# Optimization experiments

Hardware: AMD Instinct MI355X
Metric: run time of the kernel (lower is better)

Reference implementation:

```python
import jax, jax.numpy as jnp
import numpy as np

N_NODES = 50000
N_EDGES = 800000
D_IN = 128
D_OUT = 128


def setup_inputs() -> dict:
    key = jax.random.key(0)
    ks = jax.random.split(key, 6)
    x = jax.random.normal(ks[0], (N_NODES, D_IN), dtype=jnp.float32)
    edge_src = jax.random.randint(ks[1], (N_EDGES,), 0, N_NODES)
    edge_dst = jax.random.randint(ks[2], (N_EDGES,), 0, N_NODES)
    edge_val = jax.random.uniform(ks[3], (N_EDGES,), dtype=jnp.float32)
    W = jax.random.normal(ks[4], (D_OUT, D_IN), dtype=jnp.float32) / np.sqrt(D_IN)
    b = jax.random.normal(ks[5], (D_OUT,), dtype=jnp.float32) * 0.01
    return {"x": x, "edge_src": edge_src, "edge_dst": edge_dst,
            "edge_val": edge_val, "W": W, "b": b}


def reference(x, edge_src, edge_dst, edge_val, W, b):
    # h = sparse.mm(adj, x): for each edge (dst, src, val): h[dst] += val * x[src]
    msgs = edge_val[:, None] * x[edge_src]            # [E, D_IN]
    h = jax.ops.segment_sum(msgs, edge_dst, num_segments=N_NODES)  # [N, D_IN]
    # nn.Linear: h @ W.T + b, then relu activation
    out = jnp.einsum('nd,od->no', h, W) + b           # [N, D_OUT]
    return jax.nn.relu(out)
```

## Files before the change

kernel.cpp:

```cpp
#include <hip/hip_runtime.h>
#include <hip/hip_bf16.h>

#define N_NODES 50000
#define N_EDGES 800000
#define D 128
#define SCAN_NB 49

static_assert(N_NODES < 65536, "src must fit in 16 bits for epack");

typedef __attribute__((ext_vector_type(8))) short short8;
typedef __attribute__((ext_vector_type(4))) float f32x4;
typedef unsigned int uint;
typedef unsigned short ushort;

__device__ __forceinline__ ushort f2bf(float f) {
    uint u = __float_as_uint(f);
    u += 0x7fffu + ((u >> 16) & 1u);
    return (ushort)(u >> 16);
}

__device__ __forceinline__ float bflo(uint u) { return __uint_as_float(u << 16); }
__device__ __forceinline__ float bfhi(uint u) { return __uint_as_float(u & 0xffff0000u); }


__global__ __launch_bounds__(256) void sgcn_prep(
    const float* __restrict__ W, ushort* __restrict__ Wb, int* __restrict__ deg)
{
    int t = blockIdx.x * 256 + threadIdx.x;
    if (t < (D * D) / 4) {
        float4 a = reinterpret_cast<const float4*>(W)[t];
        ushort4 s;
        s.x = f2bf(a.x); s.y = f2bf(a.y); s.z = f2bf(a.z); s.w = f2bf(a.w);
        *reinterpret_cast<ushort4*>(Wb + (size_t)t * 4) = s;
    }
    if (t < N_NODES / 4) {
        reinterpret_cast<int4*>(deg)[t] = make_int4(0, 0, 0, 0);
    }
}


__global__ __launch_bounds__(256) void sgcn_hist_rank(
    const int* __restrict__ dst, int* __restrict__ deg, int* __restrict__ rank)
{
    int e = blockIdx.x * 256 + threadIdx.x;
    if (e < N_EDGES)
        rank[e] = atomicAdd(&deg[dst[e]], 1);
}

__global__ __launch_bounds__(256) void sgcn_scanf(
    const int* __restrict__ deg, int* __restrict__ rowptr)
{
    __shared__ int part[256];
    __shared__ int soff;
    int tid = threadIdx.x;
    int b = blockIdx.x;

    const int4* d4 = reinterpret_cast<const int4*>(deg);
    int pre = 0;
    for (int i = tid; i < b * 256; i += 256) {
        int4 v = d4[i];
        pre += v.x + v.y + v.z + v.w;
    }
    part[tid] = pre;
    __syncthreads();
    for (int off = 128; off > 0; off >>= 1) {
        if (tid < off) part[tid] += part[tid + off];
        __syncthreads();
    }
    if (tid == 0) soff = part[0];
    __syncthreads();

    int base = b * 1024 + tid * 4;
    int4 v = make_int4(0, 0, 0, 0);
    if (base < N_NODES) v = *reinterpret_cast<const int4*>(deg + base);
    int s = v.x + v.y + v.z + v.w;
    part[tid] = s;
    __syncthreads();
    for (int off = 1; off < 256; off <<= 1) {
        int mine  = part[tid];
        int other = (tid >= off) ? part[tid - off] : 0;
        __syncthreads();
        part[tid] = mine + other;
        __syncthreads();
    }
    int run = soff + ((tid == 0) ? 0 : part[tid - 1]);
    if (base < N_NODES) {
        int4 r;
        r.x = run;
        r.y = run + v.x;
        r.z = r.y + v.y;
        r.w = r.z + v.z;
        *reinterpret_cast<int4*>(rowptr + base) = r;
        if (base + 4 == N_NODES) rowptr[N_NODES] = r.w + v.w;
    }
}

__global__ __launch_bounds__(256) void sgcn_permute(
    const int* __restrict__ src, const int* __restrict__ dst,
    const float* __restrict__ val, const int* __restrict__ rowptr,
    const int* __restrict__ rank, uint* __restrict__ epack)
{
    int e = blockIdx.x * 256 + threadIdx.x;
    if (e < N_EDGES) {
        int pos = rowptr[dst[e]] + rank[e];
        epack[pos] = ((uint)f2bf(val[e]) << 16) | (uint)src[e];
    }
}


__global__ __launch_bounds__(256) void sgcn_gemm_y(
    const float* __restrict__ x, const ushort* __restrict__ Wb,
    ushort* __restrict__ y)
{
    int wave = threadIdx.x >> 6;
    int lane = threadIdx.x & 63;
    int lm = lane & 15;
    int kb = lane >> 4;

    short8 bfr[8][4];
#pragma unroll
    for (int nt = 0; nt < 8; ++nt)
#pragma unroll
        for (int kk = 0; kk < 4; ++kk)
            bfr[nt][kk] = *reinterpret_cast<const short8*>(
                Wb + (nt * 16 + lm) * D + kk * 32 + kb * 8);

    const int nMT = N_NODES / 16;
    int mt0 = blockIdx.x * 4 + wave;
    int strideMT = gridDim.x * 4;
    for (int mt = mt0; mt < nMT; mt += strideMT) {
        int m0 = mt * 16;
        const float* xrow = x + (long)(m0 + lm) * D + kb * 8;
        short8 afr[4];
#pragma unroll
        for (int kk = 0; kk < 4; ++kk) {
            float4 a = *reinterpret_cast<const float4*>(xrow + kk * 32);
            float4 c = *reinterpret_cast<const float4*>(xrow + kk * 32 + 4);
            short8 s;
            s[0] = (short)f2bf(a.x); s[1] = (short)f2bf(a.y);
            s[2] = (short)f2bf(a.z); s[3] = (short)f2bf(a.w);
            s[4] = (short)f2bf(c.x); s[5] = (short)f2bf(c.y);
            s[6] = (short)f2bf(c.z); s[7] = (short)f2bf(c.w);
            afr[kk] = s;
        }
#pragma unroll
        for (int nt = 0; nt < 8; ++nt) {
            f32x4 acc = {0.f, 0.f, 0.f, 0.f};
#pragma unroll
            for (int kk = 0; kk < 4; ++kk)
                acc = __builtin_amdgcn_mfma_f32_16x16x32_bf16(afr[kk], bfr[nt][kk], acc, 0, 0, 0);
            ushort* yp = y + (long)(m0 + kb * 4) * D + nt * 16 + lm;
#pragma unroll
            for (int r = 0; r < 4; ++r)
                yp[(long)r * D] = f2bf(acc[r]);
        }
    }
}


__global__ __launch_bounds__(256) void sgcn_aggregate(
    const uint* __restrict__ yb, const int* __restrict__ rowptr,
    const uint* __restrict__ ep, const float* __restrict__ bias,
    float* __restrict__ out)
{
    int n = (blockIdx.x * 256 + threadIdx.x) >> 4;
    int c = threadIdx.x & 15;
    float4 bv0 = *reinterpret_cast<const float4*>(bias + c * 8);
    float4 bv1 = *reinterpret_cast<const float4*>(bias + c * 8 + 4);

    int j0 = rowptr[n], j1 = rowptr[n + 1];
    float a0 = 0.f, a1 = 0.f, a2 = 0.f, a3 = 0.f;
    float a4 = 0.f, a5 = 0.f, a6 = 0.f, a7 = 0.f;
    int j = j0;
    for (; j + 4 <= j1; j += 4) {
        uint p0 = ep[j], p1 = ep[j + 1], p2 = ep[j + 2], p3 = ep[j + 3];
        uint4 u0 = *reinterpret_cast<const uint4*>(yb + (size_t)(p0 & 0xffffu) * 64 + c * 4);
        uint4 u1 = *reinterpret_cast<const uint4*>(yb + (size_t)(p1 & 0xffffu) * 64 + c * 4);
        uint4 u2 = *reinterpret_cast<const uint4*>(yb + (size_t)(p2 & 0xffffu) * 64 + c * 4);
        uint4 u3 = *reinterpret_cast<const uint4*>(yb + (size_t)(p3 & 0xffffu) * 64 + c * 4);
        float v0 = __uint_as_float(p0 & 0xffff0000u);
        float v1 = __uint_as_float(p1 & 0xffff0000u);
        float v2 = __uint_as_float(p2 & 0xffff0000u);
        float v3 = __uint_as_float(p3 & 0xffff0000u);
        a0 += v0 * bflo(u0.x) + v1 * bflo(u1.x) + v2 * bflo(u2.x) + v3 * bflo(u3.x);
        a1 += v0 * bfhi(u0.x) + v1 * bfhi(u1.x) + v2 * bfhi(u2.x) + v3 * bfhi(u3.x);
        a2 += v0 * bflo(u0.y) + v1 * bflo(u1.y) + v2 * bflo(u2.y) + v3 * bflo(u3.y);
        a3 += v0 * bfhi(u0.y) + v1 * bfhi(u1.y) + v2 * bfhi(u2.y) + v3 * bfhi(u3.y);
        a4 += v0 * bflo(u0.z) + v1 * bflo(u1.z) + v2 * bflo(u2.z) + v3 * bflo(u3.z);
        a5 += v0 * bfhi(u0.z) + v1 * bfhi(u1.z) + v2 * bfhi(u2.z) + v3 * bfhi(u3.z);
        a6 += v0 * bflo(u0.w) + v1 * bflo(u1.w) + v2 * bflo(u2.w) + v3 * bflo(u3.w);
        a7 += v0 * bfhi(u0.w) + v1 * bfhi(u1.w) + v2 * bfhi(u2.w) + v3 * bfhi(u3.w);
    }
    for (; j < j1; ++j) {
        uint p = ep[j];
        uint4 u = *reinterpret_cast<const uint4*>(yb + (size_t)(p & 0xffffu) * 64 + c * 4);
        float v = __uint_as_float(p & 0xffff0000u);
        a0 += v * bflo(u.x); a1 += v * bfhi(u.x);
        a2 += v * bflo(u.y); a3 += v * bfhi(u.y);
        a4 += v * bflo(u.z); a5 += v * bfhi(u.z);
        a6 += v * bflo(u.w); a7 += v * bfhi(u.w);
    }
    f32x4 r0, r1;
    r0[0] = fmaxf(a0 + bv0.x, 0.f);
    r0[1] = fmaxf(a1 + bv0.y, 0.f);
    r0[2] = fmaxf(a2 + bv0.z, 0.f);
    r0[3] = fmaxf(a3 + bv0.w, 0.f);
    r1[0] = fmaxf(a4 + bv1.x, 0.f);
    r1[1] = fmaxf(a5 + bv1.y, 0.f);
    r1[2] = fmaxf(a6 + bv1.z, 0.f);
    r1[3] = fmaxf(a7 + bv1.w, 0.f);
    f32x4* op = reinterpret_cast<f32x4*>(out + (long)n * D + c * 8);
    __builtin_nontemporal_store(r0, op);
    __builtin_nontemporal_store(r1, op + 1);
}

extern "C" void kernel_launch(void* const* d_in, const int* in_sizes, int n_in,
                              void* d_out, int out_size, void* d_ws, size_t ws_size,
                              hipStream_t stream) {
    const float* x   = (const float*)d_in[0];
    const int*   es  = (const int*)d_in[1];
    const int*   ed  = (const int*)d_in[2];
    const float* ev  = (const float*)d_in[3];
    const float* W   = (const float*)d_in[4];
    const float* b   = (const float*)d_in[5];
    float* out = (float*)d_out;

    char* ws = (char*)d_ws;
    size_t off = 0;
    uint*   yb     = (uint*)  (ws + off); off += (size_t)N_NODES * (D / 2) * sizeof(uint);
    ushort* Wb     = (ushort*)(ws + off); off += (size_t)D * D * sizeof(ushort);
    uint*   epack  = (uint*)  (ws + off); off += (size_t)N_EDGES * sizeof(uint);
    int*    rowptr = (int*)   (ws + off); off += ((size_t)(N_NODES + 1) * sizeof(int) + 15) & ~15ull;
    int*    deg    = (int*)   (ws + off); off += (size_t)N_NODES * sizeof(int);
    int* rank = (int*)d_out;

    const int EB = (N_EDGES + 255) / 256;

    sgcn_prep<<<64, 256, 0, stream>>>(W, Wb, deg);
    sgcn_gemm_y<<<512, 256, 0, stream>>>(x, Wb, (ushort*)yb);
    sgcn_hist_rank<<<EB, 256, 0, stream>>>(ed, deg, rank);
    sgcn_scanf<<<SCAN_NB, 256, 0, stream>>>(deg, rowptr);
    sgcn_permute<<<EB, 256, 0, stream>>>(es, ed, ev, rowptr, rank, epack);
    sgcn_aggregate<<<3125, 256, 0, stream>>>(yb, rowptr, epack, b, out);
}
```

Baseline: 115.9 us.

## Fuse GEMM with degree histogram in one launch and convert W in-kernel

Merges the dense x·W GEMM and the edge-degree histogram/rank atomics into a single kernel, with extra blocks doing the histogram so both run concurrently. The separate W-to-bf16 prep kernel is dropped: each GEMM block converts W itself, and deg is zeroed with a memset. Nontemporal loads are added for streaming reads of x, the edge arrays and epack. This cuts the number of launches and lets the atomic-bound and MFMA-bound work overlap, at the cost of redundant W conversion in every GEMM block.

```diff
diff --git a/kernel.cpp b/kernel.cpp
--- a/kernel.cpp
+++ b/kernel.cpp
@@ -5,6 +5,7 @@
 #define N_EDGES 800000
 #define D 128
 #define SCAN_NB 49
+#define GEMM_NB 512
 
 static_assert(N_NODES < 65536, "src must fit in 16 bits for epack");
 
@@ -23,29 +24,71 @@
 __device__ __forceinline__ float bfhi(uint u) { return __uint_as_float(u & 0xffff0000u); }
 
 
-__global__ __launch_bounds__(256) void sgcn_prep(
-    const float* __restrict__ W, ushort* __restrict__ Wb, int* __restrict__ deg)
-{
-    int t = blockIdx.x * 256 + threadIdx.x;
-    if (t < (D * D) / 4) {
-        float4 a = reinterpret_cast<const float4*>(W)[t];
-        ushort4 s;
-        s.x = f2bf(a.x); s.y = f2bf(a.y); s.z = f2bf(a.z); s.w = f2bf(a.w);
-        *reinterpret_cast<ushort4*>(Wb + (size_t)t * 4) = s;
-    }
-    if (t < N_NODES / 4) {
-        reinterpret_cast<int4*>(deg)[t] = make_int4(0, 0, 0, 0);
-    }
-}
-
-
-__global__ __launch_bounds__(256) void sgcn_hist_rank(
-    const int* __restrict__ dst, int* __restrict__ deg, int* __restrict__ rank)
-{
-    int e = blockIdx.x * 256 + threadIdx.x;
-    if (e < N_EDGES)
-        rank[e] = atomicAdd(&deg[dst[e]], 1);
-}
+__global__ __launch_bounds__(256) void sgcn_gemm_hist(
+    const float* __restrict__ x, const float* __restrict__ W,
+    const int* __restrict__ dst, int* __restrict__ deg, int* __restrict__ rank,
+    ushort* __restrict__ y)
+{
+    if (blockIdx.x >= GEMM_NB) {
+        int e = (blockIdx.x - GEMM_NB) * 256 + threadIdx.x;
+        if (e < N_EDGES)
+            rank[e] = atomicAdd(&deg[dst[e]], 1);
+        return;
+    }
+
+    int wave = threadIdx.x >> 6;
+    int lane = threadIdx.x & 63;
+    int lm = lane & 15;
+    int kb = lane >> 4;
+
+    short8 bfr[8][4];
+#pragma unroll
+    for (int nt = 0; nt < 8; ++nt)
+#pragma unroll
+        for (int kk = 0; kk < 4; ++kk) {
+            const float* wp = W + (nt * 16 + lm) * D + kk * 32 + kb * 8;
+            float4 a = *reinterpret_cast<const float4*>(wp);
+            float4 c = *reinterpret_cast<const float4*>(wp + 4);
+            short8 s;
+            s[0] = (short)f2bf(a.x); s[1] = (short)f2bf(a.y);
+            s[2] = (short)f2bf(a.z); s[3] = (short)f2bf(a.w);
+            s[4] = (short)f2bf(c.x); s[5] = (short)f2bf(c.y);
+            s[6] = (short)f2bf(c.z); s[7] = (short)f2bf(c.w);
+            bfr[nt][kk] = s;
+        }
+
+    const int nMT = N_NODES / 16;
+    int mt0 = blockIdx.x * 4 + wave;
+    int strideMT = GEMM_NB * 4;
+    for (int mt = mt0; mt < nMT; mt += strideMT) {
+        int m0 = mt * 16;
+        const float* xrow = x + (long)(m0 + lm) * D + kb * 8;
+        short8 afr[4];
+#pragma unroll
+        for (int kk = 0; kk < 4; ++kk) {
+            f32x4 a = __builtin_nontemporal_load(reinterpret_cast<const f32x4*>(xrow + kk * 32));
+            f32x4 c = __builtin_nontemporal_load(reinterpret_cast<const f32x4*>(xrow + kk * 32 + 4));
+            short8 s;
+            s[0] = (short)f2bf(a[0]); s[1] = (short)f2bf(a[1]);
+            s[2] = (short)f2bf(a[2]); s[3] = (short)f2bf(a[3]);
+            s[4] = (short)f2bf(c[0]); s[5] = (short)f2bf(c[1]);
+            s[6] = (short)f2bf(c[2]); s[7] = (short)f2bf(c[3]);
+            afr[kk] = s;
+        }
+#pragma unroll
+        for (int nt = 0; nt < 8; ++nt) {
+            f32x4 acc = {0.f, 0.f, 0.f, 0.f};
+#pragma unroll
+            for (int kk = 0; kk < 4; ++kk)
+                acc = __builtin_amdgcn_mfma_f32_16x16x32_bf16(afr[kk], bfr[nt][kk], acc, 0, 0, 0);
+            ushort* yp = y + (long)(m0 + kb * 4) * D + nt * 16 + lm;
+#pragma unroll
+            for (int r = 0; r < 4; ++r)
+                yp[(long)r * D] = f2bf(acc[r]);
+        }
+    }
+}
+
 
 __global__ __launch_bounds__(256) void sgcn_scanf(
     const int* __restrict__ deg, int* __restrict__ rowptr)
@@ -102,58 +145,12 @@
 {
     int e = blockIdx.x * 256 + threadIdx.x;
     if (e < N_EDGES) {
-        int pos = rowptr[dst[e]] + rank[e];
-        epack[pos] = ((uint)f2bf(val[e]) << 16) | (uint)src[e];
-    }
-}
-
-
-__global__ __launch_bounds__(256) void sgcn_gemm_y(
-    const float* __restrict__ x, const ushort* __restrict__ Wb,
-    ushort* __restrict__ y)
-{
-    int wave = threadIdx.x >> 6;
-    int lane = threadIdx.x & 63;
-    int lm = lane & 15;
-    int kb = lane >> 4;
-
-    short8 bfr[8][4];
-#pragma unroll
-    for (int nt = 0; nt < 8; ++nt)
-#pragma unroll
-        for (int kk = 0; kk < 4; ++kk)
-            bfr[nt][kk] = *reinterpret_cast<const short8*>(
-                Wb + (nt * 16 + lm) * D + kk * 32 + kb * 8);
-
-    const int nMT = N_NODES / 16;
-    int mt0 = blockIdx.x * 4 + wave;
-    int strideMT = gridDim.x * 4;
-    for (int mt = mt0; mt < nMT; mt += strideMT) {
-        int m0 = mt * 16;
-        const float* xrow = x + (long)(m0 + lm) * D + kb * 8;
-        short8 afr[4];
-#pragma unroll
-        for (int kk = 0; kk < 4; ++kk) {
-            float4 a = *reinterpret_cast<const float4*>(xrow + kk * 32);
-            float4 c = *reinterpret_cast<const float4*>(xrow + kk * 32 + 4);
-            short8 s;
-            s[0] = (short)f2bf(a.x); s[1] = (short)f2bf(a.y);
-            s[2] = (short)f2bf(a.z); s[3] = (short)f2bf(a.w);
-            s[4] = (short)f2bf(c.x); s[5] = (short)f2bf(c.y);
-            s[6] = (short)f2bf(c.z); s[7] = (short)f2bf(c.w);
-            afr[kk] = s;
-        }
-#pragma unroll
-        for (int nt = 0; nt < 8; ++nt) {
-            f32x4 acc = {0.f, 0.f, 0.f, 0.f};
-#pragma unroll
-            for (int kk = 0; kk < 4; ++kk)
-                acc = __builtin_amdgcn_mfma_f32_16x16x32_bf16(afr[kk], bfr[nt][kk], acc, 0, 0, 0);
-            ushort* yp = y + (long)(m0 + kb * 4) * D + nt * 16 + lm;
-#pragma unroll
-            for (int r = 0; r < 4; ++r)
-                yp[(long)r * D] = f2bf(acc[r]);
-        }
+        int d  = __builtin_nontemporal_load(dst + e);
+        int s  = __builtin_nontemporal_load(src + e);
+        float v = __builtin_nontemporal_load(val + e);
+        int rk = __builtin_nontemporal_load(rank + e);
+        int pos = rowptr[d] + rk;
+        epack[pos] = ((uint)f2bf(v) << 16) | (uint)s;
     }
 }
 
@@ -173,7 +170,10 @@
     float a4 = 0.f, a5 = 0.f, a6 = 0.f, a7 = 0.f;
     int j = j0;
     for (; j + 4 <= j1; j += 4) {
-        uint p0 = ep[j], p1 = ep[j + 1], p2 = ep[j + 2], p3 = ep[j + 3];
+        uint p0 = __builtin_nontemporal_load(ep + j);
+        uint p1 = __builtin_nontemporal_load(ep + j + 1);
+        uint p2 = __builtin_nontemporal_load(ep + j + 2);
+        uint p3 = __builtin_nontemporal_load(ep + j + 3);
         uint4 u0 = *reinterpret_cast<const uint4*>(yb + (size_t)(p0 & 0xffffu) * 64 + c * 4);
         uint4 u1 = *reinterpret_cast<const uint4*>(yb + (size_t)(p1 & 0xffffu) * 64 + c * 4);
         uint4 u2 = *reinterpret_cast<const uint4*>(yb + (size_t)(p2 & 0xffffu) * 64 + c * 4);
@@ -192,7 +192,7 @@
         a7 += v0 * bfhi(u0.w) + v1 * bfhi(u1.w) + v2 * bfhi(u2.w) + v3 * bfhi(u3.w);
     }
     for (; j < j1; ++j) {
-        uint p = ep[j];
+        uint p = __builtin_nontemporal_load(ep + j);
         uint4 u = *reinterpret_cast<const uint4*>(yb + (size_t)(p & 0xffffu) * 64 + c * 4);
         float v = __uint_as_float(p & 0xffff0000u);
         a0 += v * bflo(u.x); a1 += v * bfhi(u.x);
@@ -228,7 +228,6 @@
     char* ws = (char*)d_ws;
     size_t off = 0;
     uint*   yb     = (uint*)  (ws + off); off += (size_t)N_NODES * (D / 2) * sizeof(uint);
-    ushort* Wb     = (ushort*)(ws + off); off += (size_t)D * D * sizeof(ushort);
     uint*   epack  = (uint*)  (ws + off); off += (size_t)N_EDGES * sizeof(uint);
     int*    rowptr = (int*)   (ws + off); off += ((size_t)(N_NODES + 1) * sizeof(int) + 15) & ~15ull;
     int*    deg    = (int*)   (ws + off); off += (size_t)N_NODES * sizeof(int);
@@ -236,9 +235,8 @@
 
     const int EB = (N_EDGES + 255) / 256;
 
-    sgcn_prep<<<64, 256, 0, stream>>>(W, Wb, deg);
-    sgcn_gemm_y<<<512, 256, 0, stream>>>(x, Wb, (ushort*)yb);
-    sgcn_hist_rank<<<EB, 256, 0, stream>>>(ed, deg, rank);
+    (void)hipMemsetAsync(deg, 0, (size_t)N_NODES * sizeof(int), stream);
+    sgcn_gemm_hist<<<GEMM_NB + EB, 256, 0, stream>>>(x, W, ed, deg, rank, (ushort*)yb);
     sgcn_scanf<<<SCAN_NB, 256, 0, stream>>>(deg, rowptr);
     sgcn_permute<<<EB, 256, 0, stream>>>(es, ed, ev, rowptr, rank, epack);
     sgcn_aggregate<<<3125, 256, 0, stream>>>(yb, rowptr, epack, b, out);
```

After: 135.8 us. 1.17x slower.
